# Kernel tuning notes

Hardware: AMD Instinct MI355X
Metric: run time of the kernel (lower is better)

## Reference

```python
import jax, jax.numpy as jnp
import numpy as np

B, T, H = 64, 512, 256
D = 2 * H            # input dim to slot LSTM (bidirectional encoder repr)
MAX_SLOTS = 64       # max slot spans kept per sentence
MAX_LEN = 8          # max tokens per span
N_SLOT_TYPES = 64


def _pack_spans(bio):
    """Segment BIO tags into spans: each span = B token + following I tokens.
    Returns token index table [B, MAX_SLOTS, MAX_LEN] and validity mask."""
    bsz, t = bio.shape
    bmask = bio == 1
    imask = bio == 2
    sid = jnp.cumsum(bmask.astype(jnp.int32), axis=1) - 1      # span id per token
    valid = (bmask | imask) & (sid >= 0)
    cs = jnp.cumsum(valid.astype(jnp.int32), axis=1)           # running count of span tokens
    bi = jnp.arange(bsz)[:, None]
    # cs value at each span's B token (overflow spans dumped into slot MAX_SLOTS)
    sid_b = jnp.where(bmask & (sid < MAX_SLOTS), sid, MAX_SLOTS)
    start = jnp.zeros((bsz, MAX_SLOTS + 1), jnp.int32).at[bi, sid_b].set(cs)[:, :MAX_SLOTS]
    sid_c = jnp.clip(sid, 0, MAX_SLOTS - 1)
    rank = cs - jnp.take_along_axis(start, sid_c, axis=1)      # position within span (B token -> 0)
    ok = valid & (sid < MAX_SLOTS) & (rank < MAX_LEN)
    s_idx = jnp.where(ok, sid_c, MAX_SLOTS)
    r_idx = jnp.where(ok, rank, MAX_LEN)
    tpos = jnp.broadcast_to(jnp.arange(t, dtype=jnp.int32), (bsz, t))
    tok = jnp.zeros((bsz, MAX_SLOTS + 1, MAX_LEN + 1), jnp.int32).at[bi, s_idx, r_idx].set(tpos)
    vm = jnp.zeros((bsz, MAX_SLOTS + 1, MAX_LEN + 1), bool).at[bi, s_idx, r_idx].set(True)
    return tok[:, :MAX_SLOTS, :MAX_LEN], vm[:, :MAX_SLOTS, :MAX_LEN]


def _lstm(x, Wih, Whh, b):
    """Unidirectional LSTM. x: [N, L, D] -> outputs [N, L, H] (torch gate order i,f,g,o)."""
    xg = jnp.einsum('nld,gd->nlg', x, Wih) + b                 # [N, L, 4H]
    n, l, _ = xg.shape
    h0 = jnp.zeros((n, Whh.shape[1]), x.dtype)

    def step(carry, xt):
        h, c = carry
        g = xt + h @ Whh.T
        i, f, gg, o = jnp.split(g, 4, axis=-1)
        c = jax.nn.sigmoid(f) * c + jax.nn.sigmoid(i) * jnp.tanh(gg)
        h = jax.nn.sigmoid(o) * jnp.tanh(c)
        return (h, c), h

    _, hs = jax.lax.scan(step, (h0, h0), jnp.swapaxes(xg, 0, 1))
    return jnp.swapaxes(hs, 0, 1)


def reference(lstm_repr, W_ih_f, W_hh_f, b_f, W_ih_b, W_hh_b, b_b, slot_emb, bio):
    tok, vm = _pack_spans(bio)                                  # [B,MS,ML], [B,MS,ML]
    bi = jnp.arange(lstm_repr.shape[0])[:, None, None]
    spans = lstm_repr[bi, tok]                                  # [B,MS,ML,D]
    lens = vm.sum(-1)                                           # [B,MS]
    # reverse each span within its valid length (padding stays at the end)
    pos = jnp.arange(MAX_LEN)
    rpos = lens[..., None] - 1 - pos
    ridx = jnp.where(rpos >= 0, rpos, 0)
    spans_rev = jnp.take_along_axis(spans, ridx[..., None], axis=2)
    ms = MAX_SLOTS
    xf = spans.reshape(-1, MAX_LEN, D)
    xb = spans_rev.reshape(-1, MAX_LEN, D)
    m = vm.reshape(-1, MAX_LEN, 1).astype(lstm_repr.dtype)
    hf = _lstm(xf, W_ih_f, W_hh_f, b_f)                         # [B*MS, ML, H]
    hb = _lstm(xb, W_ih_b, W_hh_b, b_b)
    pooled = jnp.concatenate([(hf * m).sum(1), (hb * m).sum(1)], axis=-1)  # sum-pool over span
    pooled = pooled.reshape(lstm_repr.shape[0], ms, 2 * H)
    scores = jnp.einsum('bsh,kh->bsk', pooled, slot_emb)        # [B,MS,n_slot_types]
    scores = scores * (lens > 0)[..., None]
    return scores


def setup_inputs() -> dict:
    key = jax.random.key(0)
    ks = jax.random.split(key, 9)
    s = 0.05
    return {
        'lstm_repr': jax.random.normal(ks[0], (B, T, D), jnp.float32),
        'W_ih_f': jax.random.normal(ks[1], (4 * H, D), jnp.float32) * s,
        'W_hh_f': jax.random.normal(ks[2], (4 * H, H), jnp.float32) * s,
        'b_f': jax.random.normal(ks[3], (4 * H,), jnp.float32) * s,
        'W_ih_b': jax.random.normal(ks[4], (4 * H, D), jnp.float32) * s,
        'W_hh_b': jax.random.normal(ks[5], (4 * H, H), jnp.float32) * s,
        'b_b': jax.random.normal(ks[6], (4 * H,), jnp.float32) * s,
        'slot_emb': jax.random.normal(ks[7], (N_SLOT_TYPES, 2 * H), jnp.float32) * s,
        'bio': jax.random.randint(ks[8], (B, T), 0, 3, dtype=jnp.int32),
    }
```

## Files before the change

### kernel.cpp

```cpp
#include <hip/hip_runtime.h>
#include <hip/hip_bf16.h>
#include <stdint.h>

#define B_ 64
#define T_ 512
#define H_ 256
#define D_ 512
#define MS_ 64
#define ML_ 8
#define NST_ 64

typedef unsigned short u16;
typedef __bf16 bf8 __attribute__((ext_vector_type(8)));
typedef float f4 __attribute__((ext_vector_type(4)));

__device__ __forceinline__ u16 f2bf(float f) {
    unsigned u = __builtin_bit_cast(unsigned, f);
    u += 0x7fffu + ((u >> 16) & 1u);
    return (u16)(u >> 16);
}
__device__ __forceinline__ float bf2f(u16 v) {
    return __builtin_bit_cast(float, (unsigned)v << 16);
}
__device__ __forceinline__ float sigm(float x) { return 1.f / (1.f + __expf(-x)); }


__global__ __launch_bounds__(512) void pack_spans2(const int* __restrict__ bio,
                                                   int* __restrict__ tok,
                                                   int* __restrict__ lenb) {
    __shared__ int wsum[8];
    __shared__ int start_s[64];
    __shared__ int len_s[64];
    int b = blockIdx.x;
    int t = threadIdx.x;
    int lane = t & 63, w = t >> 6;
    int v = bio[b * T_ + t];
    int bm = (v == 1);
    int im = (v == 2);
    if (t < 64) len_s[t] = 0;

    int x = bm;
#pragma unroll
    for (int off = 1; off < 64; off <<= 1) {
        int y = __shfl_up(x, off, 64);
        if (lane >= off) x += y;
    }
    if (lane == 63) wsum[w] = x;
    __syncthreads();
    int wof = 0;
    for (int i = 0; i < w; ++i) wof += wsum[i];
    int sid = x + wof - 1;
    int valid = ((bm | im) && sid >= 0) ? 1 : 0;
    __syncthreads();

    x = valid;
#pragma unroll
    for (int off = 1; off < 64; off <<= 1) {
        int y = __shfl_up(x, off, 64);
        if (lane >= off) x += y;
    }
    if (lane == 63) wsum[w] = x;
    __syncthreads();
    wof = 0;
    for (int i = 0; i < w; ++i) wof += wsum[i];
    int cs = x + wof;

    if (bm && sid < MS_) start_s[sid] = cs;
    __syncthreads();

    if (valid && sid < MS_) {
        int rank = cs - start_s[sid];
        if (rank < ML_) {
            tok[(b * MS_ + sid) * ML_ + rank] = t;
            atomicAdd(&len_s[sid], 1);
        }
    }
    __syncthreads();
    if (t < 64) lenb[b * MS_ + t] = len_s[t];
}

__global__ __launch_bounds__(256) void prep(
        const float* __restrict__ wihf, const float* __restrict__ whhf,
        const float* __restrict__ wihb, const float* __restrict__ whhb,
        const float* __restrict__ bf, const float* __restrict__ bb,
        u16* __restrict__ wcx, u16* __restrict__ wch, float* __restrict__ bc,
        const float* __restrict__ repr, const int* __restrict__ tok,
        const int* __restrict__ lenb,
        int* __restrict__ lists, int* __restrict__ counts, u16* __restrict__ xg) {
    int bid = blockIdx.x, gsz = gridDim.x, tid = threadIdx.x;
    if (bid == 0) {
        __shared__ int wsum[4];
        int lane = tid & 63, w = tid >> 6;
        int len[16];
#pragma unroll
        for (int i = 0; i < 16; ++i) len[i] = lenb[tid * 16 + i];
        for (int p = 0; p < ML_; ++p) {
            int c = 0;
#pragma unroll
            for (int i = 0; i < 16; ++i) c += (len[i] > p) ? 1 : 0;
            int x = c;
#pragma unroll
            for (int off = 1; off < 64; off <<= 1) {
                int y = __shfl_up(x, off, 64);
                if (lane >= off) x += y;
            }
            if (lane == 63) wsum[w] = x;
            __syncthreads();
            int wof = 0;
            for (int i = 0; i < w; ++i) wof += wsum[i];
            int pos = wof + x - c;
#pragma unroll
            for (int i = 0; i < 16; ++i)
                if (len[i] > p) lists[p * 4096 + pos++] = tid * 16 + i;
            if (tid == 255) counts[p] = pos;
            __syncthreads();
        }
        return;
    }
    int b1 = bid - 1, g1 = gsz - 1;
    for (int ch = b1; ch < 6152; ch += g1) {
        int i = ch * 256 + tid;
        if (i < 1572864) {
            int dir = i / 786432;
            int rem = i - dir * 786432;
            int n = rem / 768;
            int k = rem - n * 768;
            int nn = n & 63, c = n >> 6;
            int orig = (nn >> 4) * 256 + c * 16 + (nn & 15);
            if (k < 512) {
                const float* wih = dir ? wihb : wihf;
                wcx[((size_t)dir * 1024 + n) * 512 + k] = f2bf(wih[orig * 512 + k]);
            } else {
                const float* whh = dir ? whhb : whhf;
                wch[((size_t)dir * 1024 + n) * 256 + (k - 512)] =
                    f2bf(whh[orig * 256 + (k - 512)]);
            }
        } else if (i < 1574912) {
            int i2 = i - 1572864;
            int dir = i2 >> 10;
            int n = i2 & 1023;
            int nn = n & 63, c = n >> 6;
            int orig = (nn >> 4) * 256 + c * 16 + (nn & 15);
            bc[i2] = (dir ? bb : bf)[orig];
        }
    }
    for (int gq = b1; gq < 8192; gq += g1) {
        int sr = gq * 4 + (tid >> 6);
        int i = tid & 63;
        int span = sr >> 3, rank = sr & 7;
        if (rank < lenb[span]) {
            int t = tok[sr];
            int b = span >> 6;
            const float4* src = (const float4*)(repr + (size_t)(b * T_ + t) * D_);
            ushort4* dst = (ushort4*)(xg + (size_t)sr * D_);
            float4 v0 = src[i * 2], v1 = src[i * 2 + 1];
            ushort4 o0, o1;
            o0.x = f2bf(v0.x); o0.y = f2bf(v0.y); o0.z = f2bf(v0.z); o0.w = f2bf(v0.w);
            o1.x = f2bf(v1.x); o1.y = f2bf(v1.y); o1.z = f2bf(v1.z); o1.w = f2bf(v1.w);
            dst[i * 2] = o0; dst[i * 2 + 1] = o1;
        }
    }
}

__global__ __launch_bounds__(256) void xgk(const u16* __restrict__ xg,
                                           const u16* __restrict__ wcx,
                                           const float* __restrict__ bc,
                                           const int* __restrict__ lenb,
                                           const int* __restrict__ lists,
                                           const int* __restrict__ counts,
                                           u16* __restrict__ xgates) {
    __shared__ __align__(16) u16 As[64 * 72];
    __shared__ __align__(16) u16 Bs[64 * 72];
    __shared__ unsigned xoffs[64];
    int tid = threadIdx.x;
    int lane = tid & 63;
    int w16 = (tid >> 6) * 16;
    int mr = lane & 15;
    int q = lane >> 4;
    int q8 = q * 8;

    int S = 0;
#pragma unroll
    for (int pp = 0; pp < 8; ++pp) S += (counts[pp] + 63) >> 6;
    int S2 = 2 * S;

    int it = blockIdx.x;
    int g = it >> 4, xs = it & 15;
    if (g >= S2) return;
    int dir = (g >= S) ? 1 : 0;
    int gg = dir ? g - S : g;
    int p = 0;
#pragma unroll
    for (int pp = 0; pp < 7; ++pp) {
        int nbp = (counts[pp] + 63) >> 6;
        bool adv = (p == pp) && (gg >= nbp);
        if (adv) { gg -= nbp; p = pp + 1; }
    }
    int rbk = gg;
    int cnt = counts[p];
    int base = rbk * 64;

    if (tid < 64) {
        unsigned xo = 0;
        int idx = base + tid;
        if (idx < cnt) {
            int span = lists[p * 4096 + idx];
            int L = lenb[span];
            int rank = dir ? (L - 1 - p) : p;
            xo = (unsigned)(span * ML_ + rank) * D_;
        }
        xoffs[tid] = xo;
    }
    __syncthreads();

    int n0 = xs * 64;
    const u16* wb = wcx + (size_t)dir * 1024 * 512;
    f4 acc[4];
    f4 zed = {0.f, 0.f, 0.f, 0.f};
#pragma unroll
    for (int i = 0; i < 4; ++i) acc[i] = zed;

    for (int kt = 0; kt < 8; ++kt) {
#pragma unroll
        for (int i = 0; i < 2; ++i) {
            int c = tid + i * 256;
            int row = c >> 3;
            int cc = (c & 7) * 8;
            *(uint4*)&As[row * 72 + cc] =
                *(const uint4*)(xg + xoffs[row] + kt * 64 + cc);
            *(uint4*)&Bs[row * 72 + cc] =
                *(const uint4*)(wb + (size_t)(n0 + row) * 512 + kt * 64 + cc);
        }
        __syncthreads();
#pragma unroll
        for (int kk = 0; kk < 64; kk += 32) {
            bf8 af = *(const bf8*)&As[(w16 + mr) * 72 + kk + q8];
#pragma unroll
            for (int nt = 0; nt < 4; ++nt) {
                bf8 bg = *(const bf8*)&Bs[(nt * 16 + mr) * 72 + kk + q8];
                acc[nt] = __builtin_amdgcn_mfma_f32_16x16x32_bf16(af, bg, acc[nt], 0, 0, 0);
            }
        }
        __syncthreads();
    }

    int y = (dir * 8 + p) * 64 + rbk;
    u16 tmp[16];
#pragma unroll
    for (int nt = 0; nt < 4; ++nt)
#pragma unroll
        for (int r = 0; r < 4; ++r) {
            int n = n0 + nt * 16 + mr;
            tmp[nt * 4 + r] = f2bf(acc[nt][r] + bc[dir * 1024 + n]);
        }
    size_t off = ((size_t)(y * 16 + xs) * 256 + tid) * 16;
    *(uint4*)&xgates[off] = *(const uint4*)tmp;
    *(uint4*)&xgates[off + 8] = *(const uint4*)(tmp + 8);
}

__global__ __launch_bounds__(256) void p0k(const u16* __restrict__ xgates,
                                           const int* __restrict__ lists,
                                           const int* __restrict__ counts,
                                           float* __restrict__ cbuf,
                                           u16* __restrict__ hout,
                                           float* __restrict__ pooled) {
    __shared__ int spans_s[64];
    int tid = threadIdx.x;
    int lane = tid & 63;
    int w16 = (tid >> 6) * 16;
    int mr = lane & 15;
    int q = lane >> 4;
    int cnt = counts[0];
    int nb0 = (cnt + 63) >> 6;
    int it = blockIdx.x;
    if (it >= 2 * nb0) return;
    int dir = it / nb0;
    int rbk = it - dir * nb0;
    int base = rbk * 64;
    if (tid < 64) {
        int span = 0;
        int idx = base + tid;
        if (idx < cnt) span = lists[idx];
        spans_s[tid] = span;
    }
    __syncthreads();
    int y = dir * 512 + rbk;
    for (int xs = 0; xs < 16; ++xs) {
        u16 tmp[16];
        const uint4* s = (const uint4*)(xgates + ((size_t)(y * 16 + xs) * 256 + tid) * 16);
        ((uint4*)tmp)[0] = s[0];
        ((uint4*)tmp)[1] = s[1];
#pragma unroll
        for (int r = 0; r < 4; ++r) {
            int m = w16 + q * 4 + r;
            if (base + m < cnt) {
                int span = spans_s[m];
                int j = xs * 16 + mr;
                float gi = bf2f(tmp[0 + r]);
                float gg = bf2f(tmp[8 + r]);
                float go = bf2f(tmp[12 + r]);
                float cn = sigm(gi) * tanhf(gg);
                float h = sigm(go) * tanhf(cn);
                int si = (dir * 4096 + span) * H_ + j;
                cbuf[si] = cn;
                hout[si] = f2bf(h);
                pooled[span * 512 + dir * H_ + j] = h;
            }
        }
    }
}

__global__ __launch_bounds__(256) void stepk(const u16* __restrict__ xgates,
                                             const u16* __restrict__ hin,
                                             u16* __restrict__ hout,
                                             const u16* __restrict__ wch,
                                             const int* __restrict__ lists,
                                             const int* __restrict__ counts,
                                             float* __restrict__ cbuf,
                                             float* __restrict__ pooled, int p) {
    __shared__ __align__(16) u16 As[64 * 72];
    __shared__ __align__(16) u16 Bs[64 * 72];
    __shared__ unsigned hoffs[64];
    __shared__ int spans_s[64];
    int tid = threadIdx.x;
    int lane = tid & 63;
    int w16 = (tid >> 6) * 16;
    int mr = lane & 15;
    int q = lane >> 4;
    int q8 = q * 8;
    int cnt = counts[p];
    int nbp = (cnt + 63) >> 6;
    int S2 = 2 * nbp;

    int it = blockIdx.x;
    int g = it >> 4, xs = it & 15;
    if (g >= S2) return;
    int dir = (g >= nbp) ? 1 : 0;
    int rbk = dir ? g - nbp : g;
    int base = rbk * 64;

    if (tid < 64) {
        int span = 0;
        int idx = base + tid;
        if (idx < cnt) span = lists[p * 4096 + idx];
        spans_s[tid] = span;
        hoffs[tid] = (unsigned)(dir * 4096 + span) * H_;
    }
    __syncthreads();

    int n0 = xs * 64;
    const u16* wb = wch + (size_t)dir * 1024 * 256;
    int y = (dir * 8 + p) * 64 + rbk;
    u16 tmp[16];
    {
        const uint4* sx = (const uint4*)(xgates + ((size_t)(y * 16 + xs) * 256 + tid) * 16);
        ((uint4*)tmp)[0] = sx[0];
        ((uint4*)tmp)[1] = sx[1];
    }
    f4 acc[4];
#pragma unroll
    for (int nt = 0; nt < 4; ++nt)
#pragma unroll
        for (int r = 0; r < 4; ++r) acc[nt][r] = bf2f(tmp[nt * 4 + r]);

    for (int kt = 0; kt < 4; ++kt) {
#pragma unroll
        for (int i = 0; i < 2; ++i) {
            int c = tid + i * 256;
            int row = c >> 3;
            int cc = (c & 7) * 8;
            *(uint4*)&As[row * 72 + cc] =
                *(const uint4*)(hin + hoffs[row] + kt * 64 + cc);
            *(uint4*)&Bs[row * 72 + cc] =
                *(const uint4*)(wb + (size_t)(n0 + row) * 256 + kt * 64 + cc);
        }
        __syncthreads();
#pragma unroll
        for (int kk = 0; kk < 64; kk += 32) {
            bf8 af = *(const bf8*)&As[(w16 + mr) * 72 + kk + q8];
#pragma unroll
            for (int nt = 0; nt < 4; ++nt) {
                bf8 bg = *(const bf8*)&Bs[(nt * 16 + mr) * 72 + kk + q8];
                acc[nt] = __builtin_amdgcn_mfma_f32_16x16x32_bf16(af, bg, acc[nt], 0, 0, 0);
            }
        }
        __syncthreads();
    }

#pragma unroll
    for (int r = 0; r < 4; ++r) {
        int m = w16 + q * 4 + r;
        if (base + m < cnt) {
            int span = spans_s[m];
            int j = xs * 16 + mr;
            float gi = acc[0][r], gf = acc[1][r], gg = acc[2][r], go = acc[3][r];
            int si = (dir * 4096 + span) * H_ + j;
            float c = cbuf[si];
            float cn = sigm(gf) * c + sigm(gi) * tanhf(gg);
            float h = sigm(go) * tanhf(cn);
            cbuf[si] = cn;
            hout[si] = f2bf(h);
            pooled[span * 512 + dir * H_ + j] += h;
        }
    }
}

__global__ __launch_bounds__(256) void scoresk(const float* __restrict__ pooled,
                                               const float* __restrict__ emb,
                                               const int* __restrict__ lenb,
                                               float* __restrict__ out) {
    __shared__ __align__(16) u16 As[64 * 72];
    __shared__ __align__(16) u16 Bs[64 * 72];
    int g = blockIdx.x;
    int tid = threadIdx.x;
    int lane = tid & 63;
    int w16 = (tid >> 6) * 16;
    int mr = lane & 15;
    int q = lane >> 4;
    int q8 = q * 8;

    f4 acc[4];
    f4 zed = {0.f, 0.f, 0.f, 0.f};
#pragma unroll
    for (int i = 0; i < 4; ++i) acc[i] = zed;

    for (int kt = 0; kt < 8; ++kt) {
#pragma unroll
        for (int i = 0; i < 2; ++i) {
            int c = tid + i * 256;
            int row = c >> 3;
            int cc = (c & 7) * 8;
            const float4* a =
                (const float4*)(pooled + (size_t)(g * 64 + row) * 512 + kt * 64 + cc);
            float4 v0 = a[0], v1 = a[1];
            ushort4 o0, o1;
            o0.x = f2bf(v0.x); o0.y = f2bf(v0.y); o0.z = f2bf(v0.z); o0.w = f2bf(v0.w);
            o1.x = f2bf(v1.x); o1.y = f2bf(v1.y); o1.z = f2bf(v1.z); o1.w = f2bf(v1.w);
            *(ushort4*)&As[row * 72 + cc] = o0;
            *(ushort4*)&As[row * 72 + cc + 4] = o1;
            const float4* b = (const float4*)(emb + (size_t)row * 512 + kt * 64 + cc);
            float4 w0 = b[0], w1 = b[1];
            ushort4 p0, p1;
            p0.x = f2bf(w0.x); p0.y = f2bf(w0.y); p0.z = f2bf(w0.z); p0.w = f2bf(w0.w);
            p1.x = f2bf(w1.x); p1.y = f2bf(w1.y); p1.z = f2bf(w1.z); p1.w = f2bf(w1.w);
            *(ushort4*)&Bs[row * 72 + cc] = p0;
            *(ushort4*)&Bs[row * 72 + cc + 4] = p1;
        }
        __syncthreads();
#pragma unroll
        for (int kk = 0; kk < 64; kk += 32) {
            bf8 af = *(const bf8*)&As[(w16 + mr) * 72 + kk + q8];
#pragma unroll
            for (int nt = 0; nt < 4; ++nt) {
                bf8 bg = *(const bf8*)&Bs[(nt * 16 + mr) * 72 + kk + q8];
                acc[nt] = __builtin_amdgcn_mfma_f32_16x16x32_bf16(af, bg, acc[nt], 0, 0, 0);
            }
        }
        __syncthreads();
    }

#pragma unroll
    for (int r = 0; r < 4; ++r) {
        int m = g * 64 + w16 + q * 4 + r;
        int ln = lenb[m];
#pragma unroll
        for (int nt = 0; nt < 4; ++nt) {
            int n = nt * 16 + mr;
            out[(size_t)m * 64 + n] = (ln > 0) ? acc[nt][r] : 0.f;
        }
    }
}


extern "C" void kernel_launch(void* const* d_in, const int* in_sizes, int n_in,
                              void* d_out, int out_size, void* d_ws, size_t ws_size,
                              hipStream_t stream) {
    const float* lstm_repr = (const float*)d_in[0];
    const float* W_ih_f = (const float*)d_in[1];
    const float* W_hh_f = (const float*)d_in[2];
    const float* b_f    = (const float*)d_in[3];
    const float* W_ih_b = (const float*)d_in[4];
    const float* W_hh_b = (const float*)d_in[5];
    const float* b_b    = (const float*)d_in[6];
    const float* slot_emb = (const float*)d_in[7];
    const int* bio      = (const int*)d_in[8];
    float* out = (float*)d_out;

    char* ws = (char*)d_ws;
    u16*  xg     = (u16*)(ws + 0);
    u16*  xgates = (u16*)(ws + 33554432);
    u16*  wcx    = (u16*)(ws + 167772160);
    u16*  wch    = (u16*)(ws + 169869312);
    float* bc    = (float*)(ws + 170917888);
    int*  tok    = (int*)(ws + 170926080);
    int*  lenb   = (int*)(ws + 171057152);
    int*  lists  = (int*)(ws + 171073536);
    int*  counts = (int*)(ws + 171204608);
    float* pooled= (float*)(ws + 171204864);
    float* cbuf  = (float*)(ws + 179593472);
    u16*  h0     = (u16*)(ws + 187982080);
    u16*  h1     = (u16*)(ws + 192176384);

    pack_spans2<<<64, 512, 0, stream>>>(bio, tok, lenb);
    prep<<<2048, 256, 0, stream>>>(W_ih_f, W_hh_f, W_ih_b, W_hh_b, b_f, b_b,
                                   wcx, wch, bc, lstm_repr, tok, lenb,
                                   lists, counts, xg);
    xgk<<<16384, 256, 0, stream>>>(xg, wcx, bc, lenb, lists, counts, xgates);
    p0k<<<128, 256, 0, stream>>>(xgates, lists, counts, cbuf, h1, pooled);
    for (int p = 1; p < 8; ++p) {
        const u16* hin = (p & 1) ? h1 : h0;
        u16* hout = (p & 1) ? h0 : h1;
        stepk<<<2048, 256, 0, stream>>>(xgates, hin, hout, wch, lists, counts,
                                        cbuf, pooled, p);
    }
    scoresk<<<64, 256, 0, stream>>>(pooled, slot_emb, lenb, out);
}
```

Baseline: 277.7 us.

## Widen xgk tiles to reuse gathered A rows across four N tiles

Each xgk block now computes 256 output gate columns instead of 64, keeping the gathered A tile in shared memory and iterating over four 64-column weight sub-tiles. The weight tile is double-buffered, so the next sub-tile's load is issued while MFMAs run on the current one. The grid shrinks fourfold, which cuts redundant gathers of the input rows. In exchange each block holds 16 accumulator vectors, raising register pressure, and has more barriers per k-step.

```diff
diff --git a/kernel.cpp b/kernel.cpp
--- a/kernel.cpp
+++ b/kernel.cpp
@@ -170,7 +170,7 @@
                                            const int* __restrict__ counts,
                                            u16* __restrict__ xgates) {
     __shared__ __align__(16) u16 As[64 * 72];
-    __shared__ __align__(16) u16 Bs[64 * 72];
+    __shared__ __align__(16) u16 Bs[2][64 * 72];
     __shared__ unsigned xoffs[64];
     int tid = threadIdx.x;
     int lane = tid & 63;
@@ -185,7 +185,7 @@
     int S2 = 2 * S;
 
     int it = blockIdx.x;
-    int g = it >> 4, xs = it & 15;
+    int g = it >> 2, xq = it & 3;
     if (g >= S2) return;
     int dir = (g >= S) ? 1 : 0;
     int gg = dir ? g - S : g;
@@ -213,49 +213,65 @@
     }
     __syncthreads();
 
-    int n0 = xs * 64;
+    int c0 = tid, c1 = tid + 256;
+    int row0 = c0 >> 3, cc0 = (c0 & 7) * 8;
+    int row1 = c1 >> 3, cc1 = (c1 & 7) * 8;
     const u16* wb = wcx + (size_t)dir * 1024 * 512;
-    f4 acc[4];
+    int nbase = xq * 256;
+
+    f4 acc[16];
     f4 zed = {0.f, 0.f, 0.f, 0.f};
 #pragma unroll
-    for (int i = 0; i < 4; ++i) acc[i] = zed;
+    for (int i = 0; i < 16; ++i) acc[i] = zed;
 
     for (int kt = 0; kt < 8; ++kt) {
-#pragma unroll
-        for (int i = 0; i < 2; ++i) {
-            int c = tid + i * 256;
-            int row = c >> 3;
-            int cc = (c & 7) * 8;
-            *(uint4*)&As[row * 72 + cc] =
-                *(const uint4*)(xg + xoffs[row] + kt * 64 + cc);
-            *(uint4*)&Bs[row * 72 + cc] =
-                *(const uint4*)(wb + (size_t)(n0 + row) * 512 + kt * 64 + cc);
-        }
+        *(uint4*)&As[row0 * 72 + cc0] = *(const uint4*)(xg + xoffs[row0] + kt * 64 + cc0);
+        *(uint4*)&As[row1 * 72 + cc1] = *(const uint4*)(xg + xoffs[row1] + kt * 64 + cc1);
+        *(uint4*)&Bs[0][row0 * 72 + cc0] =
+            *(const uint4*)(wb + (size_t)(nbase + row0) * 512 + kt * 64 + cc0);
+        *(uint4*)&Bs[0][row1 * 72 + cc1] =
+            *(const uint4*)(wb + (size_t)(nbase + row1) * 512 + kt * 64 + cc1);
         __syncthreads();
 #pragma unroll
-        for (int kk = 0; kk < 64; kk += 32) {
-            bf8 af = *(const bf8*)&As[(w16 + mr) * 72 + kk + q8];
-#pragma unroll
-            for (int nt = 0; nt < 4; ++nt) {
-                bf8 bg = *(const bf8*)&Bs[(nt * 16 + mr) * 72 + kk + q8];
-                acc[nt] = __builtin_amdgcn_mfma_f32_16x16x32_bf16(af, bg, acc[nt], 0, 0, 0);
-            }
-        }
-        __syncthreads();
+        for (int sub = 0; sub < 4; ++sub) {
+            if (sub < 3) {
+                int nb = nbase + (sub + 1) * 64;
+                *(uint4*)&Bs[(sub + 1) & 1][row0 * 72 + cc0] =
+                    *(const uint4*)(wb + (size_t)(nb + row0) * 512 + kt * 64 + cc0);
+                *(uint4*)&Bs[(sub + 1) & 1][row1 * 72 + cc1] =
+                    *(const uint4*)(wb + (size_t)(nb + row1) * 512 + kt * 64 + cc1);
+            }
+#pragma unroll
+            for (int kk = 0; kk < 64; kk += 32) {
+                bf8 af = *(const bf8*)&As[(w16 + mr) * 72 + kk + q8];
+#pragma unroll
+                for (int nt = 0; nt < 4; ++nt) {
+                    bf8 bg = *(const bf8*)&Bs[sub & 1][(nt * 16 + mr) * 72 + kk + q8];
+                    acc[sub * 4 + nt] =
+                        __builtin_amdgcn_mfma_f32_16x16x32_bf16(af, bg, acc[sub * 4 + nt],
+                                                                0, 0, 0);
+                }
+            }
+            __syncthreads();
+        }
     }
 
     int y = (dir * 8 + p) * 64 + rbk;
-    u16 tmp[16];
-#pragma unroll
-    for (int nt = 0; nt < 4; ++nt)
-#pragma unroll
-        for (int r = 0; r < 4; ++r) {
-            int n = n0 + nt * 16 + mr;
-            tmp[nt * 4 + r] = f2bf(acc[nt][r] + bc[dir * 1024 + n]);
-        }
-    size_t off = ((size_t)(y * 16 + xs) * 256 + tid) * 16;
-    *(uint4*)&xgates[off] = *(const uint4*)tmp;
-    *(uint4*)&xgates[off + 8] = *(const uint4*)(tmp + 8);
+#pragma unroll
+    for (int sub = 0; sub < 4; ++sub) {
+        int xs = xq * 4 + sub;
+        u16 tmp[16];
+#pragma unroll
+        for (int nt = 0; nt < 4; ++nt)
+#pragma unroll
+            for (int r = 0; r < 4; ++r) {
+                int n = xs * 64 + nt * 16 + mr;
+                tmp[nt * 4 + r] = f2bf(acc[sub * 4 + nt][r] + bc[dir * 1024 + n]);
+            }
+        size_t off = ((size_t)(y * 16 + xs) * 256 + tid) * 16;
+        *(uint4*)&xgates[off] = *(const uint4*)tmp;
+        *(uint4*)&xgates[off + 8] = *(const uint4*)(tmp + 8);
+    }
 }
 
 __global__ __launch_bounds__(256) void p0k(const u16* __restrict__ xgates,
@@ -505,7 +521,7 @@
     prep<<<2048, 256, 0, stream>>>(W_ih_f, W_hh_f, W_ih_b, W_hh_b, b_f, b_b,
                                    wcx, wch, bc, lstm_repr, tok, lenb,
                                    lists, counts, xg);
-    xgk<<<16384, 256, 0, stream>>>(xg, wcx, bc, lenb, lists, counts, xgates);
+    xgk<<<4096, 256, 0, stream>>>(xg, wcx, bc, lenb, lists, counts, xgates);
     p0k<<<128, 256, 0, stream>>>(xgates, lists, counts, cbuf, h1, pooled);
     for (int p = 1; p < 8; ++p) {
         const u16* hin = (p & 1) ? h1 : h0;
```

New measurement: 304.8 us. 9.8% more time.

## Fuse step-0 LSTM cell into input-gate GEMM and regroup blocks for weight reuse

Applied to the files above, without the earlier changes.

The position-0 LSTM cell update (no recurrent term) is computed directly in the epilogue of the input-projection GEMM from fp32 accumulators, removing the separate p0k kernel launch and the bf16 round-trip of step-0 gates through global memory. The block index mapping is also reordered so that 8 consecutive blocks share the same weight column tile (xs), which should improve L2 reuse of the weight slices. Step 0 now uses fp32 gates instead of bf16-rounded ones, which slightly changes numerics.

```diff
diff --git a/kernel.cpp b/kernel.cpp
--- a/kernel.cpp
+++ b/kernel.cpp
@@ -168,10 +168,14 @@
                                            const int* __restrict__ lenb,
                                            const int* __restrict__ lists,
                                            const int* __restrict__ counts,
-                                           u16* __restrict__ xgates) {
+                                           u16* __restrict__ xgates,
+                                           float* __restrict__ cbuf,
+                                           u16* __restrict__ h1,
+                                           float* __restrict__ pooled) {
     __shared__ __align__(16) u16 As[64 * 72];
     __shared__ __align__(16) u16 Bs[64 * 72];
     __shared__ unsigned xoffs[64];
+    __shared__ int spans_s[64];
     int tid = threadIdx.x;
     int lane = tid & 63;
     int w16 = (tid >> 6) * 16;
@@ -185,7 +189,8 @@
     int S2 = 2 * S;
 
     int it = blockIdx.x;
-    int g = it >> 4, xs = it & 15;
+    int qq = it >> 7, rem = it & 127, xs = rem >> 3, r8 = rem & 7;
+    int g = qq * 8 + r8;
     if (g >= S2) return;
     int dir = (g >= S) ? 1 : 0;
     int gg = dir ? g - S : g;
@@ -202,14 +207,16 @@
 
     if (tid < 64) {
         unsigned xo = 0;
+        int span = 0;
         int idx = base + tid;
         if (idx < cnt) {
-            int span = lists[p * 4096 + idx];
+            span = lists[p * 4096 + idx];
             int L = lenb[span];
             int rank = dir ? (L - 1 - p) : p;
             xo = (unsigned)(span * ML_ + rank) * D_;
         }
         xoffs[tid] = xo;
+        spans_s[tid] = span;
     }
     __syncthreads();
 
@@ -244,69 +251,39 @@
         __syncthreads();
     }
 
-    int y = (dir * 8 + p) * 64 + rbk;
-    u16 tmp[16];
+    float tf[16];
 #pragma unroll
     for (int nt = 0; nt < 4; ++nt)
 #pragma unroll
         for (int r = 0; r < 4; ++r) {
             int n = n0 + nt * 16 + mr;
-            tmp[nt * 4 + r] = f2bf(acc[nt][r] + bc[dir * 1024 + n]);
-        }
-    size_t off = ((size_t)(y * 16 + xs) * 256 + tid) * 16;
-    *(uint4*)&xgates[off] = *(const uint4*)tmp;
-    *(uint4*)&xgates[off + 8] = *(const uint4*)(tmp + 8);
-}
-
-__global__ __launch_bounds__(256) void p0k(const u16* __restrict__ xgates,
-                                           const int* __restrict__ lists,
-                                           const int* __restrict__ counts,
-                                           float* __restrict__ cbuf,
-                                           u16* __restrict__ hout,
-                                           float* __restrict__ pooled) {
-    __shared__ int spans_s[64];
-    int tid = threadIdx.x;
-    int lane = tid & 63;
-    int w16 = (tid >> 6) * 16;
-    int mr = lane & 15;
-    int q = lane >> 4;
-    int cnt = counts[0];
-    int nb0 = (cnt + 63) >> 6;
-    int it = blockIdx.x;
-    if (it >= 2 * nb0) return;
-    int dir = it / nb0;
-    int rbk = it - dir * nb0;
-    int base = rbk * 64;
-    if (tid < 64) {
-        int span = 0;
-        int idx = base + tid;
-        if (idx < cnt) span = lists[idx];
-        spans_s[tid] = span;
-    }
-    __syncthreads();
-    int y = dir * 512 + rbk;
-    for (int xs = 0; xs < 16; ++xs) {
-        u16 tmp[16];
-        const uint4* s = (const uint4*)(xgates + ((size_t)(y * 16 + xs) * 256 + tid) * 16);
-        ((uint4*)tmp)[0] = s[0];
-        ((uint4*)tmp)[1] = s[1];
+            tf[nt * 4 + r] = acc[nt][r] + bc[dir * 1024 + n];
+        }
+
+    if (p == 0) {
+        int j = xs * 16 + mr;
 #pragma unroll
         for (int r = 0; r < 4; ++r) {
             int m = w16 + q * 4 + r;
             if (base + m < cnt) {
                 int span = spans_s[m];
-                int j = xs * 16 + mr;
-                float gi = bf2f(tmp[0 + r]);
-                float gg = bf2f(tmp[8 + r]);
-                float go = bf2f(tmp[12 + r]);
-                float cn = sigm(gi) * tanhf(gg);
+                float gi = tf[0 + r], gg2 = tf[8 + r], go = tf[12 + r];
+                float cn = sigm(gi) * tanhf(gg2);
                 float h = sigm(go) * tanhf(cn);
                 int si = (dir * 4096 + span) * H_ + j;
                 cbuf[si] = cn;
-                hout[si] = f2bf(h);
+                h1[si] = f2bf(h);
                 pooled[span * 512 + dir * H_ + j] = h;
             }
         }
+    } else {
+        int y = (dir * 8 + p) * 64 + rbk;
+        u16 tmp[16];
+#pragma unroll
+        for (int i = 0; i < 16; ++i) tmp[i] = f2bf(tf[i]);
+        size_t off = ((size_t)(y * 16 + xs) * 256 + tid) * 16;
+        *(uint4*)&xgates[off] = *(const uint4*)tmp;
+        *(uint4*)&xgates[off + 8] = *(const uint4*)(tmp + 8);
     }
 }
 
@@ -505,8 +482,8 @@
     prep<<<2048, 256, 0, stream>>>(W_ih_f, W_hh_f, W_ih_b, W_hh_b, b_f, b_b,
                                    wcx, wch, bc, lstm_repr, tok, lenb,
                                    lists, counts, xg);
-    xgk<<<16384, 256, 0, stream>>>(xg, wcx, bc, lenb, lists, counts, xgates);
-    p0k<<<128, 256, 0, stream>>>(xgates, lists, counts, cbuf, h1, pooled);
+    xgk<<<16384, 256, 0, stream>>>(xg, wcx, bc, lenb, lists, counts, xgates,
+                                   cbuf, h1, pooled);
     for (int p = 1; p < 8; ++p) {
         const u16* hin = (p & 1) ? h1 : h0;
         u16* hout = (p & 1) ? h0 : h1;
```

New measurement: 243.1 us. 1.14x faster.
